# Performance work log

Hardware: AMD Instinct MI355X
Metric: run time of the kernel (lower is better)

## Reference

```python
import jax, jax.numpy as jnp
import numpy as np

B = 128          # batch
STATE = 128      # input_shape[0]
ACT = 32         # outputs_count
N = STATE + ACT  # graph nodes = inputs_count
E = 5120         # edges = N * avg_degree(32)
HID = 256        # hidden_count


def setup_inputs() -> dict:
    key = jax.random.key(0)
    ks = jax.random.split(key, 10)
    state = jax.random.normal(ks[0], (B, STATE), jnp.float32)
    action = jax.random.normal(ks[1], (B, ACT), jnp.float32)
    edge_index = jax.random.randint(ks[2], (2, E), 0, N, jnp.int64)
    # GConvSeq([N, HID, HID]) parameters (xavier-ish scale)
    W1 = jax.random.normal(ks[3], (N, HID), jnp.float32) / np.sqrt(N)
    b1 = jnp.zeros((HID,), jnp.float32)
    W2 = jax.random.normal(ks[4], (HID, HID), jnp.float32) / np.sqrt(HID)
    b2 = jnp.zeros((HID,), jnp.float32)
    # output Linear(hidden_count, input_shape[0])
    Wo = jax.random.normal(ks[5], (HID, STATE), jnp.float32) / np.sqrt(HID)
    bo = jnp.zeros((STATE,), jnp.float32)
    return {"state": state, "action": action, "edge_index": edge_index,
            "W1": W1, "b1": b1, "W2": W2, "b2": b2, "Wo": Wo, "bo": bo}


def reference(state, action, edge_index, W1, b1, W2, b2, Wo, bo):
    x = jnp.concatenate([state, action], axis=1)           # (B, N)
    src, dst = edge_index[0], edge_index[1]
    # dynamic graph mask: node i sees features of its in-neighbours (+ self)
    A = jnp.zeros((N, N), x.dtype).at[dst, src].set(1.0)
    A = A.at[jnp.arange(N), jnp.arange(N)].set(1.0)
    h = x[:, None, :] * A[None, :, :]                      # (B, N, N) masked node features
    deg = jnp.maximum(jnp.zeros((N,), x.dtype).at[dst].add(1.0), 1.0)

    def gconv(h, W, b):
        msgs = h[:, src, :]                                # (B, E, F) gather
        agg = jnp.zeros(h.shape, h.dtype).at[:, dst, :].add(msgs)  # scatter-add
        agg = agg / deg[None, :, None]                     # mean aggregation
        return jax.nn.relu(agg @ W + b)

    h = gconv(h, W1, b1)                                   # (B, N, HID)
    h = gconv(h, W2, b2)                                   # (B, N, HID)
    pooled = h.mean(axis=1)                                # (B, HID) readout
    y = pooled @ Wo + bo                                   # (B, STATE)
    return y + state
```

## Files before the change

kernel.cpp:

```cpp
#include <hip/hip_runtime.h>

#define NN 160
#define BB 128
#define HH 256
#define EE 5120
#define ST 128
#define AC 32
#define IH 80

typedef __attribute__((ext_vector_type(8))) short short8;
typedef __attribute__((ext_vector_type(4))) short bf16x4;
typedef unsigned short us;
typedef __attribute__((ext_vector_type(4))) float f32x4;

__device__ inline us f2b(float f) {
    unsigned u = __builtin_bit_cast(unsigned, f);
    unsigned r = (u + 0x7FFFu + ((u >> 16) & 1u)) >> 16;
    return (us)r;
}
__device__ inline float b2f(us h) {
    return __builtin_bit_cast(float, (unsigned)h << 16);
}

__global__ __launch_bounds__(256)
void k_pre(const int* __restrict__ ei, const float* __restrict__ W1,
           const float* __restrict__ W2, const float* __restrict__ state,
           const float* __restrict__ bo, us* __restrict__ Pb,
           us* __restrict__ Mb, us* __restrict__ W1t, us* __restrict__ W2t,
           float* __restrict__ out)
{
    const int bx = blockIdx.x, tid = threadIdx.x;
    if (bx < NN) {
        __shared__ int crow[NN];
        __shared__ unsigned abit[NN * NN / 32];
        __shared__ float invdeg;
        if (tid < NN) crow[tid] = 0;
        for (int i = tid; i < NN * NN / 32; i += 256) abit[i] = 0;
        __syncthreads();
        for (int e = tid; e < EE; e += 256) {
            int s = ei[e], d = ei[EE + e];
            int p = d * NN + s;
            atomicOr(&abit[p >> 5], 1u << (p & 31));
            if (d == bx) atomicAdd(&crow[s], 1);
        }
        if (tid < NN) {
            int p = tid * NN + tid;
            atomicOr(&abit[p >> 5], 1u << (p & 31));
        }
        __syncthreads();
        if (tid == 0) {
            int dg = 0;
            for (int j = 0; j < NN; j++) dg += crow[j];
            invdeg = 1.0f / (float)(dg < 1 ? 1 : dg);
        }
        __syncthreads();
        if (tid < NN) {
            int s = 0;
            for (int k = 0; k < NN; k++) {
                int p = k * NN + tid;
                if (abit[p >> 5] & (1u << (p & 31))) s += crow[k];
            }
            Pb[bx * NN + tid] = f2b((float)s * invdeg);
            Mb[bx * NN + tid] = f2b((float)crow[tid] * invdeg);
        }
    } else if (bx < NN + 160) {
        int idx = (bx - NN) * 256 + tid;
        int n = idx / NN, k = idx - n * NN;
        W1t[idx] = f2b(W1[k * HH + n]);
    } else if (bx < NN + 160 + 256) {
        int idx = (bx - NN - 160) * 256 + tid;
        int n = idx >> 8, k = idx & 255;
        W2t[idx] = f2b(W2[k * HH + n]);
    } else {
        int idx = (bx - NN - 160 - 256) * 256 + tid;
        out[idx] = state[idx] + bo[idx & 127];
    }
}

__global__ __launch_bounds__(1024, 4)
void k_mega(const us* __restrict__ Pb, const float* __restrict__ state,
            const float* __restrict__ action, const us* __restrict__ W1t,
            const float* __restrict__ b1, const us* __restrict__ Mb,
            const us* __restrict__ W2t, const float* __restrict__ b2,
            const float* __restrict__ Wo, float* __restrict__ out)
{
    __shared__ __align__(16) us h1s[256 * 168];
    __shared__ __align__(16) us R1[34560];
    __shared__ float xb[NN];
    us* Ys  = R1;
    us* W1s = R1 + 6400;
    us* Mbs = R1;
    us* ts  = R1 + 13440;
    float* pp  = (float*)R1;
    float* pts = (float*)(R1 + 2048);

    const int ihalf = blockIdx.x, b = blockIdx.y, i_base = ihalf * IH;
    const int tid = threadIdx.x, lane = tid & 63, w = tid >> 6;
    const int rl = lane & 15, kq = lane >> 4;
    const int wr = w >> 3, wc = w & 7;
    const int rY = tid >> 2, cY = (tid & 3) * 8;

    if (tid < NN) xb[tid] = (tid < ST) ? state[b * ST + tid]
                                       : action[b * AC + (tid - ST)];
    __syncthreads();

    for (int hh = 0; hh < 2; hh++) {
        for (int c = tid; c < 2560; c += 1024) {
            int r = c / 20, col = (c % 20) * 8;
            *(short8*)&W1s[r * 168 + col] =
                *(const short8*)&W1t[(size_t)(hh * 128 + r) * NN + col];
        }
        if (tid < 640) {
            short8 p = *(const short8*)&Pb[rY * NN + cY];
            short8 y;
#pragma unroll
            for (int u = 0; u < 8; u++)
                y[u] = (short)f2b(b2f((us)p[u]) * xb[cY + u]);
            *(short8*)&Ys[rY * 40 + cY] = y;
        }
        __syncthreads();

        f32x4 acc1[5];
#pragma unroll
        for (int f = 0; f < 5; f++) acc1[f] = f32x4{0.f, 0.f, 0.f, 0.f};

        for (int k0 = 0; k0 < NN; k0 += 32) {
            const bool nxt = (k0 + 32) < NN;
            short8 p;
            if (nxt && tid < 640)
                p = *(const short8*)&Pb[rY * NN + k0 + 32 + cY];
            short8 af[5], bv;
#pragma unroll
            for (int f = 0; f < 5; f++)
                af[f] = *(const short8*)&Ys[(wr * 80 + f * 16 + rl) * 40 + kq * 8];
            bv = *(const short8*)&W1s[(wc * 16 + rl) * 168 + k0 + kq * 8];
#pragma unroll
            for (int f = 0; f < 5; f++)
                acc1[f] = __builtin_amdgcn_mfma_f32_16x16x32_bf16(
                    af[f], bv, acc1[f], 0, 0, 0);
            __syncthreads();
            if (nxt && tid < 640) {
                short8 y;
#pragma unroll
                for (int u = 0; u < 8; u++)
                    y[u] = (short)f2b(b2f((us)p[u]) * xb[k0 + 32 + cY + u]);
                *(short8*)&Ys[rY * 40 + cY] = y;
            }
            __syncthreads();
        }
        {
            int h = hh * 128 + wc * 16 + rl;
            float bias = b1[h];
#pragma unroll
            for (int f = 0; f < 5; f++) {
                int i0 = wr * 80 + f * 16 + kq * 4;
                bf16x4 v;
#pragma unroll
                for (int r = 0; r < 4; r++) {
                    float t = acc1[f][r] + bias;
                    v[r] = (short)f2b(t > 0.f ? t : 0.f);
                }
                *(bf16x4*)&h1s[h * 168 + i0] = v;
            }
        }
    }
    __syncthreads();

    {
        for (int c = tid; c < 1600; c += 1024) {
            int r = c / 20, col = (c % 20) * 8;
            *(short8*)&Mbs[r * 168 + col] =
                *(const short8*)&Mb[(size_t)(i_base + r) * NN + col];
        }
        __syncthreads();

        f32x4 acc2[5];
#pragma unroll
        for (int j = 0; j < 5; j++) acc2[j] = f32x4{0.f, 0.f, 0.f, 0.f};

        for (int k0 = 0; k0 < NN; k0 += 32) {
            short8 a = *(const short8*)&h1s[(w * 16 + rl) * 168 + k0 + kq * 8];
            short8 bfv[5];
#pragma unroll
            for (int j = 0; j < 5; j++)
                bfv[j] = *(const short8*)&Mbs[(j * 16 + rl) * 168 + k0 + kq * 8];
#pragma unroll
            for (int j = 0; j < 5; j++)
                acc2[j] = __builtin_amdgcn_mfma_f32_16x16x32_bf16(
                    a, bfv[j], acc2[j], 0, 0, 0);
        }
        __syncthreads();
        {
            int h0 = w * 16 + kq * 4;
#pragma unroll
            for (int j = 0; j < 5; j++) {
                int ip = j * 16 + rl;
                bf16x4 v;
#pragma unroll
                for (int r = 0; r < 4; r++)
                    v[r] = (short)f2b(acc2[j][r]);
                *(bf16x4*)&ts[ip * 264 + h0] = v;
            }
        }
        __syncthreads();
    }

    f32x4 acc3[5];
#pragma unroll
    for (int f = 0; f < 5; f++) acc3[f] = f32x4{0.f, 0.f, 0.f, 0.f};

    {
        const us* w2row = W2t + (size_t)(w * 16 + rl) * HH + kq * 8;
#pragma unroll
        for (int kk = 0; kk < 8; kk++) {
            short8 bv = *(const short8*)&w2row[kk * 32];
            short8 af[5];
#pragma unroll
            for (int f = 0; f < 5; f++)
                af[f] = *(const short8*)&ts[(f * 16 + rl) * 264 + kk * 32 + kq * 8];
#pragma unroll
            for (int f = 0; f < 5; f++)
                acc3[f] = __builtin_amdgcn_mfma_f32_16x16x32_bf16(
                    af[f], bv, acc3[f], 0, 0, 0);
        }
    }
    __syncthreads();

    {
        int h = w * 16 + rl;
        float bias = b2[h];
        float s = 0.f;
#pragma unroll
        for (int f = 0; f < 5; f++)
#pragma unroll
            for (int r = 0; r < 4; r++) {
                float v = acc3[f][r] + bias;
                s += v > 0.f ? v : 0.f;
            }
        pp[kq * HH + h] = s;
    }
    __syncthreads();
    {
        const int q = tid >> 7, s2 = tid & 127;
        float part = 0.f;
        for (int hx = q * 32; hx < q * 32 + 32; hx++) {
            float ph = pp[0 * HH + hx] + pp[1 * HH + hx] +
                       pp[2 * HH + hx] + pp[3 * HH + hx];
            part += ph * Wo[hx * ST + s2];
        }
        pts[q * ST + s2] = part;
        __syncthreads();
        if (tid < ST) {
            float o = 0.f;
#pragma unroll
            for (int qq = 0; qq < 8; qq++) o += pts[qq * ST + tid];
            atomicAdd(&out[b * ST + tid], o * (1.0f / NN));
        }
    }
}

extern "C" void kernel_launch(void* const* d_in, const int* in_sizes, int n_in,
                              void* d_out, int out_size, void* d_ws, size_t ws_size,
                              hipStream_t stream) {
    const float* state  = (const float*)d_in[0];
    const float* action = (const float*)d_in[1];
    const int*   ei     = (const int*)d_in[2];
    const float* W1     = (const float*)d_in[3];
    const float* b1     = (const float*)d_in[4];
    const float* W2     = (const float*)d_in[5];
    const float* b2     = (const float*)d_in[6];
    const float* Wo     = (const float*)d_in[7];
    const float* bo     = (const float*)d_in[8];
    float* out = (float*)d_out;

    char* ws = (char*)d_ws;
    size_t off = 0;
    auto alloc = [&](size_t bytes) {
        void* p = ws + off;
        off += (bytes + 255) & ~(size_t)255;
        return p;
    };
    us* Pb  = (us*)alloc(NN * NN * 2);
    us* Mb  = (us*)alloc(NN * NN * 2);
    us* W1t = (us*)alloc((size_t)HH * NN * 2);
    us* W2t = (us*)alloc((size_t)HH * HH * 2);

    k_pre<<<NN + 160 + 256 + 64, 256, 0, stream>>>(ei, W1, W2, state, bo,
                                                   Pb, Mb, W1t, W2t, out);
    {
        dim3 g(2, BB);
        k_mega<<<g, 1024, 0, stream>>>(Pb, state, action, W1t, b1, Mb, W2t, b2,
                                       Wo, out);
    }
}
```

Baseline: 35.02 us.

## Stage full masked Y once in LDS, read W1 and Mb fragments from global

Builds the entire masked input tile Ys (160x160) in shared memory once up front, replacing the per-k-chunk rebuild that was done twice with two barriers per step. W1 and Mb fragments are now loaded straight from global memory into registers instead of being staged through LDS, and several syncthreads are removed. Shared memory is re-laid out into one region with aliasing. This trades LDS staging and barriers for more global/L2 loads per wave, and the aliasing of pp/ts with Ys must stay race-free once barriers are dropped.

Measured after the change: 33.13 us. -5.4%, faster.

```diff
diff --git a/kernel.cpp b/kernel.cpp
--- a/kernel.cpp
+++ b/kernel.cpp
@@ -84,69 +84,51 @@
             const us* __restrict__ W2t, const float* __restrict__ b2,
             const float* __restrict__ Wo, float* __restrict__ out)
 {
-    __shared__ __align__(16) us h1s[256 * 168];
-    __shared__ __align__(16) us R1[34560];
+    __shared__ __align__(16) us SH[69888];
     __shared__ float xb[NN];
-    us* Ys  = R1;
-    us* W1s = R1 + 6400;
-    us* Mbs = R1;
-    us* ts  = R1 + 13440;
-    float* pp  = (float*)R1;
-    float* pts = (float*)(R1 + 2048);
+    us* Ys  = SH;
+    us* ts  = SH;
+    us* h1s = SH + 26880;
+    float* pp  = (float*)&SH[21120];
+    float* pts = (float*)&SH[23168];
 
     const int ihalf = blockIdx.x, b = blockIdx.y, i_base = ihalf * IH;
     const int tid = threadIdx.x, lane = tid & 63, w = tid >> 6;
     const int rl = lane & 15, kq = lane >> 4;
     const int wr = w >> 3, wc = w & 7;
-    const int rY = tid >> 2, cY = (tid & 3) * 8;
 
     if (tid < NN) xb[tid] = (tid < ST) ? state[b * ST + tid]
                                        : action[b * AC + (tid - ST)];
     __syncthreads();
 
+    for (int c = tid; c < 3200; c += 1024) {
+        int r = c / 20, col = (c % 20) * 8;
+        short8 p = *(const short8*)&Pb[r * NN + col];
+        short8 y;
+#pragma unroll
+        for (int u = 0; u < 8; u++)
+            y[u] = (short)f2b(b2f((us)p[u]) * xb[col + u]);
+        *(short8*)&Ys[r * 168 + col] = y;
+    }
+    __syncthreads();
+
     for (int hh = 0; hh < 2; hh++) {
-        for (int c = tid; c < 2560; c += 1024) {
-            int r = c / 20, col = (c % 20) * 8;
-            *(short8*)&W1s[r * 168 + col] =
-                *(const short8*)&W1t[(size_t)(hh * 128 + r) * NN + col];
-        }
-        if (tid < 640) {
-            short8 p = *(const short8*)&Pb[rY * NN + cY];
-            short8 y;
-#pragma unroll
-            for (int u = 0; u < 8; u++)
-                y[u] = (short)f2b(b2f((us)p[u]) * xb[cY + u]);
-            *(short8*)&Ys[rY * 40 + cY] = y;
-        }
-        __syncthreads();
-
         f32x4 acc1[5];
 #pragma unroll
         for (int f = 0; f < 5; f++) acc1[f] = f32x4{0.f, 0.f, 0.f, 0.f};
 
-        for (int k0 = 0; k0 < NN; k0 += 32) {
-            const bool nxt = (k0 + 32) < NN;
-            short8 p;
-            if (nxt && tid < 640)
-                p = *(const short8*)&Pb[rY * NN + k0 + 32 + cY];
-            short8 af[5], bv;
-#pragma unroll
-            for (int f = 0; f < 5; f++)
-                af[f] = *(const short8*)&Ys[(wr * 80 + f * 16 + rl) * 40 + kq * 8];
-            bv = *(const short8*)&W1s[(wc * 16 + rl) * 168 + k0 + kq * 8];
+        const us* w1row = W1t + (size_t)(hh * 128 + wc * 16 + rl) * NN + kq * 8;
+#pragma unroll
+        for (int kk = 0; kk < 5; kk++) {
+            short8 bv = *(const short8*)&w1row[kk * 32];
+            short8 af[5];
+#pragma unroll
+            for (int f = 0; f < 5; f++)
+                af[f] = *(const short8*)&Ys[(wr * 80 + f * 16 + rl) * 168 + kk * 32 + kq * 8];
 #pragma unroll
             for (int f = 0; f < 5; f++)
                 acc1[f] = __builtin_amdgcn_mfma_f32_16x16x32_bf16(
                     af[f], bv, acc1[f], 0, 0, 0);
-            __syncthreads();
-            if (nxt && tid < 640) {
-                short8 y;
-#pragma unroll
-                for (int u = 0; u < 8; u++)
-                    y[u] = (short)f2b(b2f((us)p[u]) * xb[k0 + 32 + cY + u]);
-                *(short8*)&Ys[rY * 40 + cY] = y;
-            }
-            __syncthreads();
         }
         {
             int h = hh * 128 + wc * 16 + rl;
@@ -167,29 +149,22 @@
     __syncthreads();
 
     {
-        for (int c = tid; c < 1600; c += 1024) {
-            int r = c / 20, col = (c % 20) * 8;
-            *(short8*)&Mbs[r * 168 + col] =
-                *(const short8*)&Mb[(size_t)(i_base + r) * NN + col];
-        }
-        __syncthreads();
-
         f32x4 acc2[5];
 #pragma unroll
         for (int j = 0; j < 5; j++) acc2[j] = f32x4{0.f, 0.f, 0.f, 0.f};
 
-        for (int k0 = 0; k0 < NN; k0 += 32) {
-            short8 a = *(const short8*)&h1s[(w * 16 + rl) * 168 + k0 + kq * 8];
+#pragma unroll
+        for (int kk = 0; kk < 5; kk++) {
+            short8 a = *(const short8*)&h1s[(w * 16 + rl) * 168 + kk * 32 + kq * 8];
             short8 bfv[5];
 #pragma unroll
             for (int j = 0; j < 5; j++)
-                bfv[j] = *(const short8*)&Mbs[(j * 16 + rl) * 168 + k0 + kq * 8];
+                bfv[j] = *(const short8*)&Mb[(size_t)(i_base + j * 16 + rl) * NN + kk * 32 + kq * 8];
 #pragma unroll
             for (int j = 0; j < 5; j++)
                 acc2[j] = __builtin_amdgcn_mfma_f32_16x16x32_bf16(
                     a, bfv[j], acc2[j], 0, 0, 0);
         }
-        __syncthreads();
         {
             int h0 = w * 16 + kq * 4;
 #pragma unroll
@@ -202,13 +177,12 @@
                 *(bf16x4*)&ts[ip * 264 + h0] = v;
             }
         }
-        __syncthreads();
-    }
+    }
+    __syncthreads();
 
     f32x4 acc3[5];
 #pragma unroll
     for (int f = 0; f < 5; f++) acc3[f] = f32x4{0.f, 0.f, 0.f, 0.f};
-
     {
         const us* w2row = W2t + (size_t)(w * 16 + rl) * HH + kq * 8;
 #pragma unroll
@@ -224,7 +198,6 @@
                     af[f], bv, acc3[f], 0, 0, 0);
         }
     }
-    __syncthreads();
 
     {
         int h = w * 16 + rl;
```
